# Kernel optimization log

Measured on AMD Instinct MI355X. Metric: run time of the kernel, lower is better.

The kernel has to match this reference:

```python
import jax, jax.numpy as jnp
import numpy as np

DIM_IN = 1024
DIM_OUT = 1024
CTX = 2048


def setup_inputs() -> dict:
    key = jax.random.key(0)
    k_x, k_q, k_k, k_v = jax.random.split(key, 4)
    x = jax.random.normal(k_x, (4, CTX, DIM_IN), dtype=jnp.float32)
    # nn.Linear default init ~ U(-1/sqrt(fan_in), 1/sqrt(fan_in)); scale doesn't matter for correctness
    s = 1.0 / np.sqrt(DIM_IN)
    Wq = jax.random.uniform(k_q, (DIM_IN, DIM_OUT), jnp.float32, -s, s)
    Wk = jax.random.uniform(k_k, (DIM_IN, DIM_OUT), jnp.float32, -s, s)
    Wv = jax.random.uniform(k_v, (DIM_IN, DIM_OUT), jnp.float32, -s, s)
    return {"x": x, "Wq": Wq, "Wk": Wk, "Wv": Wv}


def reference(x, Wq, Wk, Wv):
    # x: [B, T, D_in]; W*: [D_in, D_out]
    b, t, _ = x.shape
    q = jnp.einsum('btd,de->bte', x, Wq)
    k = jnp.einsum('btd,de,->bte', x, Wk, jnp.float32(1.0)) if False else jnp.einsum('btd,de->bte', x, Wk)
    v = jnp.einsum('btd,de->bte', x, Wv)
    scores = jnp.einsum('bqe,bke->bqk', q, k)  # [B, T, T]
    causal = jnp.tril(jnp.ones((t, t), dtype=bool))  # True where allowed
    scores = jnp.where(causal, scores, -jnp.inf)
    weights = jax.nn.softmax(scores / jnp.sqrt(jnp.float32(k.shape[-1])), axis=-1)
    # dropout p=0.0 -> identity
    return jnp.einsum('bqk,bke->bqe', weights, v)
```

## Files before the change

kernel.cpp:

```cpp
#include <hip/hip_runtime.h>


using f32x4 = __attribute__((ext_vector_type(4))) float;
using s16x8 = __attribute__((ext_vector_type(8))) short;

#define CTX 2048
#define DIM 1024
#define NB 4

__device__ __forceinline__ short f2bf(float f) {
  union { float f; unsigned u; } v; v.f = f;
  unsigned r = (v.u + 0x7fffu + ((v.u >> 16) & 1u)) >> 16;
  return (short)r;
}

__device__ __forceinline__ void async16(const void* g, void* l) {
  __builtin_amdgcn_global_load_lds(
      (const __attribute__((address_space(1))) void*)g,
      (__attribute__((address_space(3))) void*)l, 16, 0, 0);
}


__global__ __launch_bounds__(256) void cvt_x(const float* __restrict__ in,
                                             short* __restrict__ out, long n8) {
  long i = (long)blockIdx.x * 256 + threadIdx.x;
  if (i >= n8) return;
  const float4* p = (const float4*)in;
  float4 a = p[i * 2], b = p[i * 2 + 1];
  short o[8];
  o[0] = f2bf(a.x); o[1] = f2bf(a.y); o[2] = f2bf(a.z); o[3] = f2bf(a.w);
  o[4] = f2bf(b.x); o[5] = f2bf(b.y); o[6] = f2bf(b.z); o[7] = f2bf(b.w);
  *(int4*)&out[i * 8] = *(int4*)o;
}

__global__ __launch_bounds__(256) void cvt_wT(const float* __restrict__ Wq,
                                              const float* __restrict__ Wk,
                                              const float* __restrict__ Wv,
                                              short* __restrict__ WT) {
  int z = blockIdx.z;
  const float* W = (z == 0) ? Wq : (z == 1) ? Wk : Wv;
  short* o = WT + (long)z * DIM * DIM;
  __shared__ float t[32][33];
  int n0 = blockIdx.x * 32, k0 = blockIdx.y * 32;
  int tx = threadIdx.x, ty = threadIdx.y;
  #pragma unroll
  for (int j = 0; j < 4; ++j)
    t[ty + j * 8][tx] = W[(long)(k0 + ty + j * 8) * DIM + n0 + tx];
  __syncthreads();
  #pragma unroll
  for (int j = 0; j < 4; ++j)
    o[(long)(n0 + ty + j * 8) * DIM + k0 + tx] = f2bf(t[tx][ty + j * 8]);
}

#define READ_A(mh)                                                              \
  do {                                                                          \
    _Pragma("unroll") for (int mi = 0; mi < 4; ++mi) {                          \
      _Pragma("unroll") for (int ks = 0; ks < 2; ++ks) {                        \
        aA[mi][ks] = *(const s16x8*)(smem + abase + laneRd +                    \
                                     ((mh)*4 + mi) * 2048 + ks * 64);           \
      }                                                                         \
    }                                                                           \
  } while (0)

#define READ_B(nh)                                                              \
  do {                                                                          \
    _Pragma("unroll") for (int ni = 0; ni < 2; ++ni) {                          \
      _Pragma("unroll") for (int ks = 0; ks < 2; ++ks) {                        \
        bB[ni][ks] = *(const s16x8*)(smem + bbase + laneRd +                    \
                                     ((nh)*2 + ni) * 2048 + ks * 64);           \
      }                                                                         \
    }                                                                           \
  } while (0)

#define DO_MFMA(mh, nh)                                                         \
  do {                                                                          \
    __builtin_amdgcn_s_setprio(1);                                              \
    _Pragma("unroll") for (int mi = 0; mi < 4; ++mi) {                          \
      _Pragma("unroll") for (int ni = 0; ni < 2; ++ni) {                        \
        _Pragma("unroll") for (int ks = 0; ks < 2; ++ks) {                      \
          acc[(mh)*4 + mi][(nh)*2 + ni] = __builtin_amdgcn_mfma_f32_16x16x32_bf16( \
              aA[mi][ks], bB[ni][ks], acc[(mh)*4 + mi][(nh)*2 + ni], 0, 0, 0);  \
        }                                                                       \
      }                                                                         \
    }                                                                           \
    __builtin_amdgcn_s_setprio(0);                                              \
  } while (0)

template <int MODE, bool CSKIP, bool KLIM, bool SWZGRID>
__global__ __launch_bounds__(512, 1) void gemm256(const short* __restrict__ A,
                                                  const short* __restrict__ B,
                                                  void* __restrict__ Cout,
                                                  int K, long sA, long sB, long sC,
                                                  int ldc, int nbx) {
  int bx, by;
  if (SWZGRID) {
    int wg = ((int)blockIdx.x & 7) * ((int)gridDim.x >> 3) + ((int)blockIdx.x >> 3);
    bx = wg % nbx; by = wg / nbx;
  } else {
    bx = blockIdx.x; by = blockIdx.y;
  }
  const int bz = blockIdx.z;
  if (CSKIP && by > bx) return;

  const short* Ab = A + bz * sA + (long)bx * 256 * K;
  const short* Bb = B + bz * sB + (long)by * 256 * K;
  const long ldb = (long)K * 2;

  __shared__ __align__(16) char smem[131072];

  const int tid = threadIdx.x;
  const int lane = tid & 63, wid = tid >> 6;
  const int wm = wid >> 2, wn = wid & 3;
  const int frow = lane & 15, kgrp = lane >> 4;
  const int xorv = ((frow >> 2) & 1) << 5;
  const int laneRd = frow * 128 + ((kgrp * 16) ^ xorv);
  const int sr0 = tid >> 3;
  const int scb = ((tid & 7) << 4) ^ (((tid >> 5) & 1) << 5);

  int kt_end = K >> 6;
  if (KLIM) { int lim = (bx + 1) << 2; if (lim < kt_end) kt_end = lim; }

  f32x4 acc[8][4];
  const f32x4 zero = {0.f, 0.f, 0.f, 0.f};
  #pragma unroll
  for (int mi = 0; mi < 8; ++mi)
    #pragma unroll
    for (int ni = 0; ni < 4; ++ni) acc[mi][ni] = zero;

  auto STAGE = [&](int bn_, int mat, int tt) {
    const char* mb = (const char*)(mat ? Bb : Ab) + (long)tt * 128 + scb;
    #pragma unroll
    for (int h = 0; h < 2; ++h)
      #pragma unroll
      for (int s = 0; s < 2; ++s)
        async16(mb + (long)(h * 128 + s * 64 + sr0) * ldb,
                smem + ((bn_ * 2 + mat) * 2 + h) * 16384 + s * 8192 + tid * 16);
  };

  STAGE(0, 0, 0);
  STAGE(0, 1, 0);
  asm volatile("s_waitcnt vmcnt(0)" ::: "memory");
  __builtin_amdgcn_s_barrier();

  s16x8 aA[4][2], bB[2][2];
  for (int t = 0; t < kt_end; ++t) {
    const int buf = t & 1;
    const int abase = ((buf * 2 + 0) * 2 + wm) * 16384;
    const int bbase = ((buf * 2 + 1) * 2 + (wn >> 1)) * 16384 + (wn & 1) * 8192;
    const int bn = buf ^ 1;
    const bool hn = (t + 1 < kt_end);

    if (hn) STAGE(bn, 0, t + 1);
    READ_A(0); READ_B(0);
    __builtin_amdgcn_s_barrier();
    DO_MFMA(0, 0);

    if (hn) STAGE(bn, 1, t + 1);
    READ_A(1);
    __builtin_amdgcn_s_barrier();
    DO_MFMA(1, 0);

    READ_B(1);
    __builtin_amdgcn_s_barrier();
    DO_MFMA(1, 1);

    READ_A(0);
    __builtin_amdgcn_s_barrier();
    DO_MFMA(0, 1);

    asm volatile("s_waitcnt vmcnt(0)" ::: "memory");
    __builtin_amdgcn_s_barrier();
  }

  const int row0 = bx * 256 + wm * 128;
  const int col0 = by * 256 + wn * 64;
  #pragma unroll
  for (int mi = 0; mi < 8; ++mi) {
    #pragma unroll
    for (int ni = 0; ni < 4; ++ni) {
      #pragma unroll
      for (int r = 0; r < 4; ++r) {
        const int row = row0 + mi * 16 + kgrp * 4 + r;
        const int col = col0 + ni * 16 + frow;
        const float v = acc[mi][ni][r];
        if (MODE == 2) {
          ((_Float16*)Cout)[bz * sC + (long)row * ldc + col] = (_Float16)v;
        } else if (MODE == 3) {
          ((float*)Cout)[bz * sC + (long)row * ldc + col] = v;
        } else {
          const long QK = (long)NB * CTX * DIM;
          const int colr = col & 1023;
          long off;
          if (col < 2048) {
            off = (long)(col >> 10) * QK + (long)row * DIM + colr;
          } else {
            off = 2 * QK + (long)(row >> 11) * ((long)DIM * CTX) +
                  (long)colr * CTX + (row & (CTX - 1));
          }
          ((short*)Cout)[off] = f2bf(v);
        }
      }
    }
  }
}

__global__ __launch_bounds__(256) void softmax_causal(void* __restrict__ Sbuf) {
  const int r = blockIdx.x, b = blockIdx.y;
  const long base = (long)b * CTX * CTX + (long)r * CTX;
  _Float16* S = (_Float16*)Sbuf + base;
  short* P = (short*)Sbuf + base;
  const int tid = threadIdx.x;
  const int lane = tid & 63, wid = tid >> 6;
  const int c0 = tid * 8;
  const int ncol = ((r >> 8) + 1) << 8;
  const float scale = 0.03125f;

  float v[8];
  if (c0 <= r) {
    _Float16 h[8];
    *(int4*)h = *(const int4*)&S[c0];
    #pragma unroll
    for (int j = 0; j < 8; ++j)
      v[j] = (c0 + j <= r) ? (float)h[j] * scale : -INFINITY;
  } else {
    #pragma unroll
    for (int j = 0; j < 8; ++j) v[j] = -INFINITY;
  }
  float m = -INFINITY;
  #pragma unroll
  for (int j = 0; j < 8; ++j) m = fmaxf(m, v[j]);
  #pragma unroll
  for (int off = 32; off >= 1; off >>= 1) m = fmaxf(m, __shfl_xor(m, off));
  __shared__ float redm[4], reds[4];
  if (lane == 0) redm[wid] = m;
  __syncthreads();
  m = fmaxf(fmaxf(redm[0], redm[1]), fmaxf(redm[2], redm[3]));

  float p[8];
  float s = 0.f;
  #pragma unroll
  for (int j = 0; j < 8; ++j) {
    p[j] = exp2f((v[j] - m) * 1.44269504f);
    s += p[j];
  }
  #pragma unroll
  for (int off = 32; off >= 1; off >>= 1) s += __shfl_xor(s, off);
  if (lane == 0) reds[wid] = s;
  __syncthreads();
  s = reds[0] + reds[1] + reds[2] + reds[3];
  const float inv = 1.0f / s;

  if (c0 < ncol) {
    short o[8];
    #pragma unroll
    for (int j = 0; j < 8; ++j) o[j] = f2bf(p[j] * inv);
    *(int4*)&P[c0] = *(int4*)o;
  }
}

extern "C" void kernel_launch(void* const* d_in, const int* in_sizes, int n_in,
                              void* d_out, int out_size, void* d_ws, size_t ws_size,
                              hipStream_t stream) {
  (void)in_sizes; (void)n_in; (void)out_size; (void)ws_size;
  const float* x  = (const float*)d_in[0];
  const float* Wq = (const float*)d_in[1];
  const float* Wk = (const float*)d_in[2];
  const float* Wv = (const float*)d_in[3];

  const long MB = 1024 * 1024;
  char* ws = (char*)d_ws;
  short* xb = (short*)(ws + 0);
  short* WT = (short*)(ws + 16 * MB);
  short* Qb = (short*)(ws + 24 * MB);
  short* Kb = (short*)(ws + 40 * MB);
  short* Vt = (short*)(ws + 56 * MB);
  void*  S  = (void*)(ws + 72 * MB);

  cvt_x<<<4096, 256, 0, stream>>>(x, xb, (long)NB * CTX * DIM / 8);
  cvt_wT<<<dim3(32, 32, 3), dim3(32, 8), 0, stream>>>(Wq, Wk, Wv, WT);
  gemm256<4, false, false, true><<<384, 512, 0, stream>>>(
      xb, WT, Qb, DIM, 0, 0, 0, DIM, 32);
  gemm256<2, true, false, false><<<dim3(8, 8, NB), 512, 0, stream>>>(
      Qb, Kb, S, DIM, (long)CTX * DIM, (long)CTX * DIM, (long)CTX * CTX, CTX, 0);
  softmax_causal<<<dim3(CTX, NB), 256, 0, stream>>>(S);
  gemm256<3, false, true, false><<<dim3(8, 4, NB), 512, 0, stream>>>(
      (short*)S, Vt, d_out, CTX, (long)CTX * CTX, (long)DIM * CTX, (long)CTX * DIM, DIM, 0);
}
```

Before: 309.6 us.

## Restructure GEMM mainloop into 4-slot half-K pipeline with new LDS layout

Replaces the double-buffered 64-wide K tile loop with a four-slot ring of 32-wide K half-tiles, prefetching three slots ahead and waiting with vmcnt(4) instead of draining all loads each iteration. The LDS layout changes from a row-major XOR-swizzled tile to a k-group-major layout, so each lane's fragment reads are contiguous 16-byte chunks, and the MFMA phases are regrouped into two N-halves per half-tile. The grid swizzle for the projection GEMM is hardcoded into 8x6 groups. The aim is deeper load/compute overlap and fewer full memory drains, at the cost of a new, unswizzled LDS pattern that could cause bank conflicts and more barriers per K step.

```diff
diff --git a/kernel.cpp b/kernel.cpp
--- a/kernel.cpp
+++ b/kernel.cpp
@@ -19,6 +19,13 @@
       (const __attribute__((address_space(1))) void*)g,
       (__attribute__((address_space(3))) void*)l, 16, 0, 0);
 }
+
+#define FENCE_BAR()                              \
+  do {                                           \
+    asm volatile("" ::: "memory");               \
+    __builtin_amdgcn_s_barrier();                \
+    asm volatile("" ::: "memory");               \
+  } while (0)
 
 
 __global__ __launch_bounds__(256) void cvt_x(const float* __restrict__ in,
@@ -52,38 +59,16 @@
     o[(long)(n0 + ty + j * 8) * DIM + k0 + tx] = f2bf(t[tx][ty + j * 8]);
 }
 
-#define READ_A(mh)                                                              \
-  do {                                                                          \
-    _Pragma("unroll") for (int mi = 0; mi < 4; ++mi) {                          \
-      _Pragma("unroll") for (int ks = 0; ks < 2; ++ks) {                        \
-        aA[mi][ks] = *(const s16x8*)(smem + abase + laneRd +                    \
-                                     ((mh)*4 + mi) * 2048 + ks * 64);           \
-      }                                                                         \
-    }                                                                           \
-  } while (0)
-
-#define READ_B(nh)                                                              \
-  do {                                                                          \
-    _Pragma("unroll") for (int ni = 0; ni < 2; ++ni) {                          \
-      _Pragma("unroll") for (int ks = 0; ks < 2; ++ks) {                        \
-        bB[ni][ks] = *(const s16x8*)(smem + bbase + laneRd +                    \
-                                     ((nh)*2 + ni) * 2048 + ks * 64);           \
-      }                                                                         \
-    }                                                                           \
-  } while (0)
-
-#define DO_MFMA(mh, nh)                                                         \
-  do {                                                                          \
-    __builtin_amdgcn_s_setprio(1);                                              \
-    _Pragma("unroll") for (int mi = 0; mi < 4; ++mi) {                          \
-      _Pragma("unroll") for (int ni = 0; ni < 2; ++ni) {                        \
-        _Pragma("unroll") for (int ks = 0; ks < 2; ++ks) {                      \
-          acc[(mh)*4 + mi][(nh)*2 + ni] = __builtin_amdgcn_mfma_f32_16x16x32_bf16( \
-              aA[mi][ks], bB[ni][ks], acc[(mh)*4 + mi][(nh)*2 + ni], 0, 0, 0);  \
-        }                                                                       \
-      }                                                                         \
-    }                                                                           \
-    __builtin_amdgcn_s_setprio(0);                                              \
+#define MFMA_PHASE(nh)                                                       \
+  do {                                                                       \
+    __builtin_amdgcn_s_setprio(1);                                           \
+    _Pragma("unroll") for (int mi = 0; mi < 8; ++mi) {                       \
+      _Pragma("unroll") for (int ni = 0; ni < 2; ++ni) {                     \
+        acc[mi][(nh) * 2 + ni] = __builtin_amdgcn_mfma_f32_16x16x32_bf16(    \
+            aA[mi], bB[ni], acc[mi][(nh) * 2 + ni], 0, 0, 0);                \
+      }                                                                      \
+    }                                                                        \
+    __builtin_amdgcn_s_setprio(0);                                           \
   } while (0)
 
 template <int MODE, bool CSKIP, bool KLIM, bool SWZGRID>
@@ -91,19 +76,20 @@
                                                   const short* __restrict__ B,
                                                   void* __restrict__ Cout,
                                                   int K, long sA, long sB, long sC,
-                                                  int ldc, int nbx) {
+                                                  int ldc) {
   int bx, by;
   if (SWZGRID) {
-    int wg = ((int)blockIdx.x & 7) * ((int)gridDim.x >> 3) + ((int)blockIdx.x >> 3);
-    bx = wg % nbx; by = wg / nbx;
+    const int j = (int)blockIdx.x & 7, i = (int)blockIdx.x >> 3;
+    bx = (j & 3) * 8 + (i & 7);
+    by = (j >> 2) * 6 + (i >> 3);
   } else {
     bx = blockIdx.x; by = blockIdx.y;
   }
   const int bz = blockIdx.z;
   if (CSKIP && by > bx) return;
 
-  const short* Ab = A + bz * sA + (long)bx * 256 * K;
-  const short* Bb = B + bz * sB + (long)by * 256 * K;
+  const char* Ab = (const char*)(A + bz * sA + (long)bx * 256 * K);
+  const char* Bb = (const char*)(B + bz * sB + (long)by * 256 * K);
   const long ldb = (long)K * 2;
 
   __shared__ __align__(16) char smem[131072];
@@ -112,13 +98,15 @@
   const int lane = tid & 63, wid = tid >> 6;
   const int wm = wid >> 2, wn = wid & 3;
   const int frow = lane & 15, kgrp = lane >> 4;
-  const int xorv = ((frow >> 2) & 1) << 5;
-  const int laneRd = frow * 128 + ((kgrp * 16) ^ xorv);
-  const int sr0 = tid >> 3;
-  const int scb = ((tid & 7) << 4) ^ (((tid >> 5) & 1) << 5);
+
+  const long soff0 = (long)(tid & 255) * ldb + ((tid >> 8) << 4);
+  const int sdst = tid * 16;
+  const int aoff = kgrp * 4096 + (wm * 128 + frow) * 16;
+  const int boff = 65536 + kgrp * 4096 + (wn * 64 + frow) * 16;
 
   int kt_end = K >> 6;
   if (KLIM) { int lim = (bx + 1) << 2; if (lim < kt_end) kt_end = lim; }
+  const int HK = kt_end * 2;
 
   f32x4 acc[8][4];
   const f32x4 zero = {0.f, 0.f, 0.f, 0.f};
@@ -127,49 +115,48 @@
     #pragma unroll
     for (int ni = 0; ni < 4; ++ni) acc[mi][ni] = zero;
 
-  auto STAGE = [&](int bn_, int mat, int tt) {
-    const char* mb = (const char*)(mat ? Bb : Ab) + (long)tt * 128 + scb;
-    #pragma unroll
-    for (int h = 0; h < 2; ++h)
-      #pragma unroll
-      for (int s = 0; s < 2; ++s)
-        async16(mb + (long)(h * 128 + s * 64 + sr0) * ldb,
-                smem + ((bn_ * 2 + mat) * 2 + h) * 16384 + s * 8192 + tid * 16);
+  auto STAGE = [&](int mat, int h) {
+    const char* src = (mat ? Bb : Ab) + soff0 + h * 64;
+    char* dst = (char*)smem + mat * 65536 + (h & 3) * 16384 + sdst;
+    async16(src, dst);
+    async16(src + 32, dst + 8192);
   };
 
-  STAGE(0, 0, 0);
-  STAGE(0, 1, 0);
-  asm volatile("s_waitcnt vmcnt(0)" ::: "memory");
-  __builtin_amdgcn_s_barrier();
-
-  s16x8 aA[4][2], bB[2][2];
+  STAGE(0, 0); STAGE(1, 0); STAGE(0, 1); STAGE(1, 1); STAGE(0, 2); STAGE(1, 2);
+  asm volatile("s_waitcnt vmcnt(4)" ::: "memory");
+  FENCE_BAR();
+
+  s16x8 aA[8], bB[2];
   for (int t = 0; t < kt_end; ++t) {
-    const int buf = t & 1;
-    const int abase = ((buf * 2 + 0) * 2 + wm) * 16384;
-    const int bbase = ((buf * 2 + 1) * 2 + (wn >> 1)) * 16384 + (wn & 1) * 8192;
-    const int bn = buf ^ 1;
-    const bool hn = (t + 1 < kt_end);
-
-    if (hn) STAGE(bn, 0, t + 1);
-    READ_A(0); READ_B(0);
-    __builtin_amdgcn_s_barrier();
-    DO_MFMA(0, 0);
-
-    if (hn) STAGE(bn, 1, t + 1);
-    READ_A(1);
-    __builtin_amdgcn_s_barrier();
-    DO_MFMA(1, 0);
-
-    READ_B(1);
-    __builtin_amdgcn_s_barrier();
-    DO_MFMA(1, 1);
-
-    READ_A(0);
-    __builtin_amdgcn_s_barrier();
-    DO_MFMA(0, 1);
-
-    asm volatile("s_waitcnt vmcnt(0)" ::: "memory");
-    __builtin_amdgcn_s_barrier();
+    #pragma unroll
+    for (int ks = 0; ks < 2; ++ks) {
+      const int h = 2 * t + ks;
+      const int sa = (h & 3) << 14;
+      const int hs = 2 * t + 3 + ks;
+
+      if (hs < HK) STAGE(0, hs);
+      #pragma unroll
+      for (int mi = 0; mi < 8; ++mi)
+        aA[mi] = *(const s16x8*)(smem + sa + aoff + mi * 256);
+      #pragma unroll
+      for (int ni = 0; ni < 2; ++ni)
+        bB[ni] = *(const s16x8*)(smem + sa + boff + ni * 256);
+      FENCE_BAR();
+      MFMA_PHASE(0);
+      FENCE_BAR();
+
+      if (hs < HK) STAGE(1, hs);
+      #pragma unroll
+      for (int ni = 0; ni < 2; ++ni)
+        bB[ni] = *(const s16x8*)(smem + sa + boff + 512 + ni * 256);
+      FENCE_BAR();
+      MFMA_PHASE(1);
+      if (ks == 1) {
+        if (t >= kt_end - 2) asm volatile("s_waitcnt vmcnt(0)" ::: "memory");
+        else                 asm volatile("s_waitcnt vmcnt(4)" ::: "memory");
+      }
+      FENCE_BAR();
+    }
   }
 
   const int row0 = bx * 256 + wm * 128;
@@ -279,10 +266,10 @@
   cvt_x<<<4096, 256, 0, stream>>>(x, xb, (long)NB * CTX * DIM / 8);
   cvt_wT<<<dim3(32, 32, 3), dim3(32, 8), 0, stream>>>(Wq, Wk, Wv, WT);
   gemm256<4, false, false, true><<<384, 512, 0, stream>>>(
-      xb, WT, Qb, DIM, 0, 0, 0, DIM, 32);
+      xb, WT, Qb, DIM, 0, 0, 0, DIM);
   gemm256<2, true, false, false><<<dim3(8, 8, NB), 512, 0, stream>>>(
-      Qb, Kb, S, DIM, (long)CTX * DIM, (long)CTX * DIM, (long)CTX * CTX, CTX, 0);
+      Qb, Kb, S, DIM, (long)CTX * DIM, (long)CTX * DIM, (long)CTX * CTX, CTX);
   softmax_causal<<<dim3(CTX, NB), 256, 0, stream>>>(S);
   gemm256<3, false, true, false><<<dim3(8, 4, NB), 512, 0, stream>>>(
-      (short*)S, Vt, d_out, CTX, (long)CTX * CTX, (long)DIM * CTX, (long)CTX * DIM, DIM, 0);
-}
+      (short*)S, Vt, d_out, CTX, (long)CTX * CTX, (long)DIM * CTX, (long)CTX * DIM, DIM);
+}
```

Result: slower. 345.1 us (+11.5%).
